# Kernel tuning notes

Measured on AMD Instinct MI355X. Metric: run time of the kernel, lower is better.

The kernel has to match this reference:

```python
import jax, jax.numpy as jnp
import numpy as np

B, N, T, D = 4, 170, 96, 256
H, HD = 8, 32          # num_heads, head_dim
TD, HIST, P = 24, 3, 16  # traffic_dim, history_size, num_patterns


def setup_inputs() -> dict:
    key = jax.random.key(0)
    ks = jax.random.split(key, 15)
    s = 0.02
    return {
        "query": jax.random.normal(ks[0], (B, N, T, D), jnp.float32),
        "key": jax.random.normal(ks[1], (B, N, T, D), jnp.float32),
        "value": jax.random.normal(ks[2], (B, N, T, D), jnp.float32),
        "pattern_matrix": jax.random.normal(ks[3], (P, HIST, TD), jnp.float32),
        "Wp": jax.random.normal(ks[4], (TD, TD), jnp.float32) * s,
        "bp": jnp.zeros((TD,), jnp.float32),
        "Wq": jax.random.normal(ks[5], (D, D), jnp.float32) * s,
        "bq": jnp.zeros((D,), jnp.float32),
        "Wk": jax.random.normal(ks[6], (D, D), jnp.float32) * s,
        "bk": jnp.zeros((D,), jnp.float32),
        "Wv": jax.random.normal(ks[7], (D, D), jnp.float32) * s,
        "bv": jnp.zeros((D,), jnp.float32),
        "Wo": jax.random.normal(ks[8], (D, D), jnp.float32) * s,
        "bo": jnp.zeros((D,), jnp.float32),
    }


def _forward(query, key, value, pattern_matrix, Wp, bp, Wq, bq, Wk, bk, Wv, bv, Wo, bo):
    b, n, t, d = query.shape
    # ---- compute_similarity: sliding windows over the traffic features ----
    tf = query[..., :TD]  # [B,N,T,TD]
    L = t - HIST + 1
    # windows[b,n,l,j,c] = tf[b,n,l+j,c]  (same as F.unfold with kernel (HIST,1))
    windows = jnp.stack([tf[:, :, j:j + L, :] for j in range(HIST)], axis=3)  # [B,N,L,HIST,TD]
    history_pattern = pattern_matrix @ Wp.T + bp  # [P,HIST,TD]
    # einsum('bhd,phd->bph') then mean over h == einsum over d, sum over h / HIST
    sim = jnp.einsum('bnlhd,phd->bnlp', windows, history_pattern) / HIST  # [B,N,L,P]
    pad = (HIST - 1) // 2
    sim = jnp.pad(sim, ((0, 0), (0, 0), (pad, pad), (0, 0)))  # [B,N,T,P]

    # ---- generate_temporal_mask ----
    sim_mean = sim.mean(axis=1)  # [B,T,P]
    temporal_weights = jax.nn.softmax(sim_mean, axis=-1).sum(axis=-1, keepdims=True)  # [B,T,1]
    tmask = temporal_weights @ jnp.swapaxes(temporal_weights, 1, 2)  # [B,T,T]
    # expand to [B,H,N,T,T] then flatten (torch indexing: b*H+h)
    mask_flat = jnp.broadcast_to(tmask[:, None, None, :, :], (b, H, n, t, t)).reshape(b * H, n, t, t)

    # ---- projections + head split (torch split/cat -> head-major batch: h*B+b) ----
    q = query @ Wq.T + bq
    k = key @ Wk.T + bk
    v = value @ Wv.T + bv
    def split_heads(x):
        return x.reshape(b, n, t, H, HD).transpose(3, 0, 1, 2, 4).reshape(H * b, n, t, HD)
    q, k, v = split_heads(q), split_heads(k), split_heads(v)

    scores = jnp.einsum('anqd,ankd->anqk', q, k) / jnp.sqrt(jnp.float32(HD))  # [H*B,N,T,T]
    scores = scores * mask_flat  # elementwise (shapes match; torch mixes head/batch order the same way)
    attn = jax.nn.softmax(scores, axis=-1)  # dropout is identity in eval mode
    out = jnp.einsum('anqk,ankd->anqd', attn, v)  # [H*B,N,T,HD]
    out = out.reshape(H, b, n, t, HD).transpose(1, 2, 3, 0, 4).reshape(b, n, t, d)
    return out @ Wo.T + bo


def reference(query, key, value, pattern_matrix, Wp, bp, Wq, bq, Wk, bk, Wv, bv, Wo, bo):
    return _forward(query, key, value, pattern_matrix, Wp, bp, Wq, bq, Wk, bk, Wv, bv, Wo, bo)
```

## Files before the change

### kernel.cpp

```cpp
#include <hip/hip_runtime.h>
#include <math.h>

#define B_  4
#define N_  170
#define T_  96
#define D_  256
#define H_  8
#define HD_ 32
#define BN_ (B_*N_)
#define WSZ (D_*D_)

typedef short  bf16x8 __attribute__((ext_vector_type(8)));
typedef float  f32x4  __attribute__((ext_vector_type(4)));

#define XB   0
#define KB   49152
#define VB   98304
#define LDSZ 147456

__device__ __forceinline__ ushort to_bf16(float x)
{
    uint u = __builtin_bit_cast(uint, x);
    u += 0x8000u;
    return (ushort)(u >> 16);
}

__device__ __forceinline__ uint pack2(float x0, float x1)
{
    return (uint)to_bf16(x0) | ((uint)to_bf16(x1) << 16);
}

__device__ __forceinline__ uint4 pack8(float4 a0, float4 a1)
{
    uint4 r;
    r.x = pack2(a0.x, a0.y); r.y = pack2(a0.z, a0.w);
    r.z = pack2(a1.x, a1.y); r.w = pack2(a1.z, a1.w);
    return r;
}

#define MFMA(a, b, c) __builtin_amdgcn_mfma_f32_16x16x32_bf16((a), (b), (c), 0, 0, 0)

__global__ __launch_bounds__(256)
void splitw_kernel(const float* __restrict__ Wq, const float* __restrict__ Wk,
                   const float* __restrict__ Wv, const float* __restrict__ Wo,
                   ushort* __restrict__ whi)
{
    const int gid = blockIdx.x * 256 + threadIdx.x;
    const int mat = gid >> 13;
    const int rem = gid & 8191;
    const int col = rem >> 5;
    const int kc  = rem & 31;
    const float* W = (mat == 0) ? Wq : (mat == 1) ? Wk : (mat == 2) ? Wv : Wo;
    const float s  = (mat == 0) ? 0.17677669529663687f : 1.0f;
    const float* p = W + (size_t)col * D_ + kc * 8;
    float4 a0 = *(const float4*)p;
    float4 a1 = *(const float4*)(p + 4);
    a0.x *= s; a0.y *= s; a0.z *= s; a0.w *= s;
    a1.x *= s; a1.y *= s; a1.z *= s; a1.w *= s;
    const size_t off = (size_t)mat * WSZ + ((size_t)kc * 256 + col) * 8;
    *(uint4*)(whi + off) = pack8(a0, a1);
}

__global__ __launch_bounds__(1024)
void mega_kernel(const float* __restrict__ Xq, const float* __restrict__ Xk,
                 const float* __restrict__ Xv, const ushort* __restrict__ W,
                 const float* __restrict__ bq, const float* __restrict__ bk,
                 const float* __restrict__ bv, const float* __restrict__ bo,
                 float* __restrict__ out)
{
    __shared__ __align__(16) char lds[LDSZ];

    const int bn   = blockIdx.x;
    const int tid  = threadIdx.x;
    const int wv   = tid >> 6;
    const int lane = tid & 63;
    const int lr   = lane & 15;
    const int kgl  = lane >> 4;
    const int h    = wv >> 1;
    const int ib   = (wv & 1) * 3;
    const size_t xoff = (size_t)bn * T_ * D_;

    int srow[3], skc[3]; uint saddr[3];
    #pragma unroll
    for (int c = 0; c < 3; c++) {
        const int cc = tid + c * 1024;
        const int row = cc % 96, kc = cc / 96;
        srow[c] = row; skc[c] = kc;
        saddr[c] = (uint)(((((kc >> 2) * 6 + (row >> 4)) * 4 + (kc & 3)) * 256)
                          + (row & 15) * 16);
    }

    #pragma unroll
    for (int c = 0; c < 3; c++) {
        const float* p = Xq + xoff + srow[c] * D_ + skc[c] * 8;
        float4 a0 = *(const float4*)p, a1 = *(const float4*)(p + 4);
        *(uint4*)(lds + XB + saddr[c]) = pack8(a0, a1);
    }
    __syncthreads();

    float4 pf[6];
    #pragma unroll
    for (int c = 0; c < 3; c++) {
        const float* p = Xk + xoff + srow[c] * D_ + skc[c] * 8;
        pf[2*c] = *(const float4*)p; pf[2*c+1] = *(const float4*)(p + 4);
    }

    {
        bf16x8 wf[8];
        #pragma unroll
        for (int ks = 0; ks < 8; ks++)
            wf[ks] = *(const bf16x8*)(W + ((size_t)(ks*4+kgl)*256 + wv*16 + lr)*8);
        f32x4 acc[6];
        #pragma unroll
        for (int nt = 0; nt < 6; nt++) acc[nt] = (f32x4)0.f;
        #pragma unroll
        for (int ks = 0; ks < 8; ks++)
            #pragma unroll
            for (int nt = 0; nt < 6; nt++) {
                bf16x8 xb = *(const bf16x8*)(lds + XB + ((ks*6+nt)*4+kgl)*256 + lr*16);
                acc[nt] = MFMA(wf[ks], xb, acc[nt]);
            }
        const float qs = 0.17677669529663687f;
        const int kg = (wv & 1)*2 + (kgl >> 1);
        float4 b4 = *(const float4*)(bq + wv*16 + kgl*4);
        #pragma unroll
        for (int nt = 0; nt < 6; nt++) {
            ushort4 o;
            o.x = to_bf16(acc[nt][0] + b4.x*qs);
            o.y = to_bf16(acc[nt][1] + b4.y*qs);
            o.z = to_bf16(acc[nt][2] + b4.z*qs);
            o.w = to_bf16(acc[nt][3] + b4.w*qs);
            *(ushort4*)(lds + VB + ((h*6+nt)*4+kg)*256 + lr*16 + (kgl&1)*8) = o;
        }
    }
    __syncthreads();

    #pragma unroll
    for (int c = 0; c < 3; c++)
        *(uint4*)(lds + XB + saddr[c]) = pack8(pf[2*c], pf[2*c+1]);
    bf16x8 qf[3];
    #pragma unroll
    for (int j = 0; j < 3; j++)
        qf[j] = *(const bf16x8*)(lds + VB + ((h*6 + ib + j)*4 + kgl)*256 + lr*16);
    #pragma unroll
    for (int c = 0; c < 3; c++) {
        const float* p = Xv + xoff + srow[c] * D_ + skc[c] * 8;
        pf[2*c] = *(const float4*)p; pf[2*c+1] = *(const float4*)(p + 4);
    }
    __syncthreads();

    {
        const ushort* Wk = W + WSZ;
        bf16x8 wf[8];
        #pragma unroll
        for (int ks = 0; ks < 8; ks++)
            wf[ks] = *(const bf16x8*)(Wk + ((size_t)(ks*4+kgl)*256 + wv*16 + lr)*8);
        f32x4 acc[6];
        #pragma unroll
        for (int nt = 0; nt < 6; nt++) acc[nt] = (f32x4)0.f;
        #pragma unroll
        for (int ks = 0; ks < 8; ks++)
            #pragma unroll
            for (int nt = 0; nt < 6; nt++) {
                bf16x8 xb = *(const bf16x8*)(lds + XB + ((ks*6+nt)*4+kgl)*256 + lr*16);
                acc[nt] = MFMA(wf[ks], xb, acc[nt]);
            }
        const int kg = (wv & 1)*2 + (kgl >> 1);
        float4 b4 = *(const float4*)(bk + wv*16 + kgl*4);
        #pragma unroll
        for (int nt = 0; nt < 6; nt++) {
            ushort4 o;
            o.x = to_bf16(acc[nt][0] + b4.x);
            o.y = to_bf16(acc[nt][1] + b4.y);
            o.z = to_bf16(acc[nt][2] + b4.z);
            o.w = to_bf16(acc[nt][3] + b4.w);
            *(ushort4*)(lds + KB + ((h*6+nt)*4+kg)*256 + lr*16 + (kgl&1)*8) = o;
        }
    }
    __syncthreads();

    #pragma unroll
    for (int c = 0; c < 3; c++)
        *(uint4*)(lds + XB + saddr[c]) = pack8(pf[2*c], pf[2*c+1]);
    __syncthreads();

    {
        const ushort* Wv = W + 2*WSZ;
        bf16x8 wf[8];
        #pragma unroll
        for (int ks = 0; ks < 8; ks++)
            wf[ks] = *(const bf16x8*)(Wv + ((size_t)(ks*4+kgl)*256 + wv*16 + lr)*8);
        f32x4 av[6];
        #pragma unroll
        for (int mt = 0; mt < 6; mt++) av[mt] = (f32x4)0.f;
        #pragma unroll
        for (int ks = 0; ks < 8; ks++)
            #pragma unroll
            for (int mt = 0; mt < 6; mt++) {
                bf16x8 xa = *(const bf16x8*)(lds + XB + ((ks*6+mt)*4+kgl)*256 + lr*16);
                av[mt] = MFMA(xa, wf[ks], av[mt]);
            }
        const int n2v = wv & 1;
        const float bvv = bv[wv*16 + lr];
        #pragma unroll
        for (int mt = 0; mt < 6; mt++) {
            const int kvkg = mt*2 + (kgl >> 1);
            const int s2 = kvkg >> 2, kgv = kvkg & 3;
            ushort4 o;
            o.x = to_bf16(av[mt][0] + bvv);
            o.y = to_bf16(av[mt][1] + bvv);
            o.z = to_bf16(av[mt][2] + bvv);
            o.w = to_bf16(av[mt][3] + bvv);
            *(ushort4*)(lds + VB + (((h*3+s2)*2+n2v)*4+kgv)*256 + lr*16 + (kgl&1)*8) = o;
        }
    }
    __syncthreads();

    f32x4 oacc[3][2];
    #pragma unroll
    for (int j = 0; j < 3; j++) { oacc[j][0] = (f32x4)0.f; oacc[j][1] = (f32x4)0.f; }
    {
        char* sw = lds + XB + wv * 3072;
        #pragma unroll
        for (int j = 0; j < 3; j++) {
            f32x4 s[6];
            #pragma unroll
            for (int mt = 0; mt < 6; mt++) {
                bf16x8 kf = *(const bf16x8*)(lds + KB + ((h*6+mt)*4+kgl)*256 + lr*16);
                s[mt] = MFMA(kf, qf[j], (f32x4)0.f);
            }
            float mx = s[0][0];
            #pragma unroll
            for (int mt = 0; mt < 6; mt++)
                #pragma unroll
                for (int r = 0; r < 4; r++) mx = fmaxf(mx, s[mt][r]);
            mx = fmaxf(mx, __shfl_xor(mx, 16));
            mx = fmaxf(mx, __shfl_xor(mx, 32));
            float sum = 0.f;
            #pragma unroll
            for (int mt = 0; mt < 6; mt++)
                #pragma unroll
                for (int r = 0; r < 4; r++) {
                    float e = __expf(s[mt][r] - mx);
                    s[mt][r] = e; sum += e;
                }
            sum += __shfl_xor(sum, 16);
            sum += __shfl_xor(sum, 32);
            const float inv = 1.f / sum;
            #pragma unroll
            for (int mt = 0; mt < 6; mt++) {
                uint2 u2;
                u2.x = pack2(s[mt][0]*inv, s[mt][1]*inv);
                u2.y = pack2(s[mt][2]*inv, s[mt][3]*inv);
                *(uint2*)(sw + (mt*2 + (kgl>>1))*256 + lr*16 + (kgl&1)*8) = u2;
            }
            #pragma unroll
            for (int s2 = 0; s2 < 3; s2++) {
                bf16x8 pa = *(const bf16x8*)(sw + (s2*4+kgl)*256 + lr*16);
                #pragma unroll
                for (int n2 = 0; n2 < 2; n2++) {
                    bf16x8 vf = *(const bf16x8*)(lds + VB + (((h*3+s2)*2+n2)*4+kgl)*256 + lr*16);
                    oacc[j][n2] = MFMA(pa, vf, oacc[j][n2]);
                }
            }
        }
    }
    __syncthreads();

    #pragma unroll
    for (int j = 0; j < 3; j++)
        #pragma unroll
        for (int n2 = 0; n2 < 2; n2++) {
            const int dcol = h*32 + n2*16 + lr;
            const int kc   = dcol >> 3;
            const int irow = ib + j;
            char* base = lds + XB + (((kc>>2)*6 + irow)*4 + (kc&3))*256 + (dcol&7)*2;
            #pragma unroll
            for (int r = 0; r < 4; r++)
                *(ushort*)(base + (kgl*4+r)*16) = to_bf16(oacc[j][n2][r]);
        }
    __syncthreads();

    {
        const ushort* Wo = W + 3*WSZ;
        bf16x8 wf[8];
        #pragma unroll
        for (int ks = 0; ks < 8; ks++)
            wf[ks] = *(const bf16x8*)(Wo + ((size_t)(ks*4+kgl)*256 + wv*16 + lr)*8);
        f32x4 a2[6];
        #pragma unroll
        for (int mt = 0; mt < 6; mt++) a2[mt] = (f32x4)0.f;
        #pragma unroll
        for (int ks = 0; ks < 8; ks++)
            #pragma unroll
            for (int mt = 0; mt < 6; mt++) {
                bf16x8 oa = *(const bf16x8*)(lds + XB + ((ks*6+mt)*4+kgl)*256 + lr*16);
                a2[mt] = MFMA(oa, wf[ks], a2[mt]);
            }
        const float bod = bo[wv*16 + lr];
        #pragma unroll
        for (int mt = 0; mt < 6; mt++)
            #pragma unroll
            for (int r = 0; r < 4; r++) {
                const int t = mt*16 + kgl*4 + r;
                out[((size_t)(bn*T_ + t))*D_ + wv*16 + lr] = a2[mt][r] + bod;
            }
    }
}

extern "C" void kernel_launch(void* const* d_in, const int* in_sizes, int n_in,
                              void* d_out, int out_size, void* d_ws, size_t ws_size,
                              hipStream_t stream)
{
    const float* query = (const float*)d_in[0];
    const float* key   = (const float*)d_in[1];
    const float* value = (const float*)d_in[2];
    const float* Wq = (const float*)d_in[6];
    const float* bq = (const float*)d_in[7];
    const float* Wk = (const float*)d_in[8];
    const float* bk = (const float*)d_in[9];
    const float* Wv = (const float*)d_in[10];
    const float* bv = (const float*)d_in[11];
    const float* Wo = (const float*)d_in[12];
    const float* bo = (const float*)d_in[13];

    float*  out = (float*)d_out;
    ushort* whi = (ushort*)d_ws;

    splitw_kernel<<<dim3(128), 256, 0, stream>>>(Wq, Wk, Wv, Wo, whi);
    mega_kernel<<<dim3(BN_), 1024, 0, stream>>>(
        query, key, value, whi, bq, bk, bv, bo, out);
}
```

Measured before the change: 101.6 us.

## Retile projection GEMMs into 2x3 per-wave blocks and hoist K fragments

Each wave now computes a 32-column by 48-row block (two weight column tiles times three row tiles) instead of a 16-column by 96-row strip in all four projection GEMMs. Every LDS activation fragment is reused for two MFMAs, which halves LDS reads per MFMA. In exchange the global weight fragments are reloaded per k-step instead of preloaded as eight registers. The attention stage also hoists the six K fragments out of the query-tile loop so they are read from LDS once instead of three times.

Result: slower. 111.8 us (+10.0%).

```diff
diff --git a/kernel.cpp b/kernel.cpp
--- a/kernel.cpp
+++ b/kernel.cpp
@@ -76,8 +76,9 @@
     const int lane = tid & 63;
     const int lr   = lane & 15;
     const int kgl  = lane >> 4;
-    const int h    = wv >> 1;
-    const int ib   = (wv & 1) * 3;
+    const int dp   = wv >> 1;
+    const int th   = wv & 1;
+    const int ib   = th * 3;
     const size_t xoff = (size_t)bn * T_ * D_;
 
     int srow[3], skc[3]; uint saddr[3];
@@ -106,31 +107,38 @@
     }
 
     {
-        bf16x8 wf[8];
-        #pragma unroll
-        for (int ks = 0; ks < 8; ks++)
-            wf[ks] = *(const bf16x8*)(W + ((size_t)(ks*4+kgl)*256 + wv*16 + lr)*8);
-        f32x4 acc[6];
-        #pragma unroll
-        for (int nt = 0; nt < 6; nt++) acc[nt] = (f32x4)0.f;
-        #pragma unroll
-        for (int ks = 0; ks < 8; ks++)
-            #pragma unroll
-            for (int nt = 0; nt < 6; nt++) {
-                bf16x8 xb = *(const bf16x8*)(lds + XB + ((ks*6+nt)*4+kgl)*256 + lr*16);
-                acc[nt] = MFMA(wf[ks], xb, acc[nt]);
-            }
+        f32x4 acc[2][3];
+        #pragma unroll
+        for (int u = 0; u < 2; u++)
+            #pragma unroll
+            for (int v = 0; v < 3; v++) acc[u][v] = (f32x4)0.f;
+        #pragma unroll
+        for (int ks = 0; ks < 8; ks++) {
+            bf16x8 w0 = *(const bf16x8*)(W + ((size_t)(ks*4+kgl)*256 + (dp*2+0)*16 + lr)*8);
+            bf16x8 w1 = *(const bf16x8*)(W + ((size_t)(ks*4+kgl)*256 + (dp*2+1)*16 + lr)*8);
+            #pragma unroll
+            for (int v = 0; v < 3; v++) {
+                bf16x8 xb = *(const bf16x8*)(lds + XB + ((ks*6 + th*3 + v)*4+kgl)*256 + lr*16);
+                acc[0][v] = MFMA(w0, xb, acc[0][v]);
+                acc[1][v] = MFMA(w1, xb, acc[1][v]);
+            }
+        }
         const float qs = 0.17677669529663687f;
-        const int kg = (wv & 1)*2 + (kgl >> 1);
-        float4 b4 = *(const float4*)(bq + wv*16 + kgl*4);
-        #pragma unroll
-        for (int nt = 0; nt < 6; nt++) {
-            ushort4 o;
-            o.x = to_bf16(acc[nt][0] + b4.x*qs);
-            o.y = to_bf16(acc[nt][1] + b4.y*qs);
-            o.z = to_bf16(acc[nt][2] + b4.z*qs);
-            o.w = to_bf16(acc[nt][3] + b4.w*qs);
-            *(ushort4*)(lds + VB + ((h*6+nt)*4+kg)*256 + lr*16 + (kgl&1)*8) = o;
+        #pragma unroll
+        for (int u = 0; u < 2; u++) {
+            const int mt = dp*2 + u;
+            const int kg = u*2 + (kgl >> 1);
+            float4 b4 = *(const float4*)(bq + mt*16 + kgl*4);
+            #pragma unroll
+            for (int v = 0; v < 3; v++) {
+                const int nt = th*3 + v;
+                ushort4 o;
+                o.x = to_bf16(acc[u][v][0] + b4.x*qs);
+                o.y = to_bf16(acc[u][v][1] + b4.y*qs);
+                o.z = to_bf16(acc[u][v][2] + b4.z*qs);
+                o.w = to_bf16(acc[u][v][3] + b4.w*qs);
+                *(ushort4*)(lds + VB + ((dp*6+nt)*4+kg)*256 + lr*16 + (kgl&1)*8) = o;
+            }
         }
     }
     __syncthreads();
@@ -141,7 +149,7 @@
     bf16x8 qf[3];
     #pragma unroll
     for (int j = 0; j < 3; j++)
-        qf[j] = *(const bf16x8*)(lds + VB + ((h*6 + ib + j)*4 + kgl)*256 + lr*16);
+        qf[j] = *(const bf16x8*)(lds + VB + ((dp*6 + ib + j)*4 + kgl)*256 + lr*16);
     #pragma unroll
     for (int c = 0; c < 3; c++) {
         const float* p = Xv + xoff + srow[c] * D_ + skc[c] * 8;
@@ -151,30 +159,37 @@
 
     {
         const ushort* Wk = W + WSZ;
-        bf16x8 wf[8];
-        #pragma unroll
-        for (int ks = 0; ks < 8; ks++)
-            wf[ks] = *(const bf16x8*)(Wk + ((size_t)(ks*4+kgl)*256 + wv*16 + lr)*8);
-        f32x4 acc[6];
-        #pragma unroll
-        for (int nt = 0; nt < 6; nt++) acc[nt] = (f32x4)0.f;
-        #pragma unroll
-        for (int ks = 0; ks < 8; ks++)
-            #pragma unroll
-            for (int nt = 0; nt < 6; nt++) {
-                bf16x8 xb = *(const bf16x8*)(lds + XB + ((ks*6+nt)*4+kgl)*256 + lr*16);
-                acc[nt] = MFMA(wf[ks], xb, acc[nt]);
-            }
-        const int kg = (wv & 1)*2 + (kgl >> 1);
-        float4 b4 = *(const float4*)(bk + wv*16 + kgl*4);
-        #pragma unroll
-        for (int nt = 0; nt < 6; nt++) {
-            ushort4 o;
-            o.x = to_bf16(acc[nt][0] + b4.x);
-            o.y = to_bf16(acc[nt][1] + b4.y);
-            o.z = to_bf16(acc[nt][2] + b4.z);
-            o.w = to_bf16(acc[nt][3] + b4.w);
-            *(ushort4*)(lds + KB + ((h*6+nt)*4+kg)*256 + lr*16 + (kgl&1)*8) = o;
+        f32x4 acc[2][3];
+        #pragma unroll
+        for (int u = 0; u < 2; u++)
+            #pragma unroll
+            for (int v = 0; v < 3; v++) acc[u][v] = (f32x4)0.f;
+        #pragma unroll
+        for (int ks = 0; ks < 8; ks++) {
+            bf16x8 w0 = *(const bf16x8*)(Wk + ((size_t)(ks*4+kgl)*256 + (dp*2+0)*16 + lr)*8);
+            bf16x8 w1 = *(const bf16x8*)(Wk + ((size_t)(ks*4+kgl)*256 + (dp*2+1)*16 + lr)*8);
+            #pragma unroll
+            for (int v = 0; v < 3; v++) {
+                bf16x8 xb = *(const bf16x8*)(lds + XB + ((ks*6 + th*3 + v)*4+kgl)*256 + lr*16);
+                acc[0][v] = MFMA(w0, xb, acc[0][v]);
+                acc[1][v] = MFMA(w1, xb, acc[1][v]);
+            }
+        }
+        #pragma unroll
+        for (int u = 0; u < 2; u++) {
+            const int mt = dp*2 + u;
+            const int kg = u*2 + (kgl >> 1);
+            float4 b4 = *(const float4*)(bk + mt*16 + kgl*4);
+            #pragma unroll
+            for (int v = 0; v < 3; v++) {
+                const int nt = th*3 + v;
+                ushort4 o;
+                o.x = to_bf16(acc[u][v][0] + b4.x);
+                o.y = to_bf16(acc[u][v][1] + b4.y);
+                o.z = to_bf16(acc[u][v][2] + b4.z);
+                o.w = to_bf16(acc[u][v][3] + b4.w);
+                *(ushort4*)(lds + KB + ((dp*6+nt)*4+kg)*256 + lr*16 + (kgl&1)*8) = o;
+            }
         }
     }
     __syncthreads();
@@ -186,32 +201,37 @@
 
     {
         const ushort* Wv = W + 2*WSZ;
-        bf16x8 wf[8];
-        #pragma unroll
-        for (int ks = 0; ks < 8; ks++)
-            wf[ks] = *(const bf16x8*)(Wv + ((size_t)(ks*4+kgl)*256 + wv*16 + lr)*8);
-        f32x4 av[6];
-        #pragma unroll
-        for (int mt = 0; mt < 6; mt++) av[mt] = (f32x4)0.f;
-        #pragma unroll
-        for (int ks = 0; ks < 8; ks++)
-            #pragma unroll
-            for (int mt = 0; mt < 6; mt++) {
-                bf16x8 xa = *(const bf16x8*)(lds + XB + ((ks*6+mt)*4+kgl)*256 + lr*16);
-                av[mt] = MFMA(xa, wf[ks], av[mt]);
-            }
-        const int n2v = wv & 1;
-        const float bvv = bv[wv*16 + lr];
-        #pragma unroll
-        for (int mt = 0; mt < 6; mt++) {
-            const int kvkg = mt*2 + (kgl >> 1);
-            const int s2 = kvkg >> 2, kgv = kvkg & 3;
-            ushort4 o;
-            o.x = to_bf16(av[mt][0] + bvv);
-            o.y = to_bf16(av[mt][1] + bvv);
-            o.z = to_bf16(av[mt][2] + bvv);
-            o.w = to_bf16(av[mt][3] + bvv);
-            *(ushort4*)(lds + VB + (((h*3+s2)*2+n2v)*4+kgv)*256 + lr*16 + (kgl&1)*8) = o;
+        f32x4 av[2][3];
+        #pragma unroll
+        for (int u = 0; u < 2; u++)
+            #pragma unroll
+            for (int v = 0; v < 3; v++) av[u][v] = (f32x4)0.f;
+        #pragma unroll
+        for (int ks = 0; ks < 8; ks++) {
+            bf16x8 w0 = *(const bf16x8*)(Wv + ((size_t)(ks*4+kgl)*256 + (dp*2+0)*16 + lr)*8);
+            bf16x8 w1 = *(const bf16x8*)(Wv + ((size_t)(ks*4+kgl)*256 + (dp*2+1)*16 + lr)*8);
+            #pragma unroll
+            for (int v = 0; v < 3; v++) {
+                bf16x8 xa = *(const bf16x8*)(lds + XB + ((ks*6 + th*3 + v)*4+kgl)*256 + lr*16);
+                av[0][v] = MFMA(xa, w0, av[0][v]);
+                av[1][v] = MFMA(xa, w1, av[1][v]);
+            }
+        }
+        #pragma unroll
+        for (int u = 0; u < 2; u++) {
+            const float bvv = bv[(dp*2+u)*16 + lr];
+            #pragma unroll
+            for (int v = 0; v < 3; v++) {
+                const int mt = th*3 + v;
+                const int kvkg = mt*2 + (kgl >> 1);
+                const int s2 = kvkg >> 2, kgv = kvkg & 3;
+                ushort4 o;
+                o.x = to_bf16(av[u][v][0] + bvv);
+                o.y = to_bf16(av[u][v][1] + bvv);
+                o.z = to_bf16(av[u][v][2] + bvv);
+                o.w = to_bf16(av[u][v][3] + bvv);
+                *(ushort4*)(lds + VB + (((dp*3+s2)*2+u)*4+kgv)*256 + lr*16 + (kgl&1)*8) = o;
+            }
         }
     }
     __syncthreads();
@@ -221,14 +241,16 @@
     for (int j = 0; j < 3; j++) { oacc[j][0] = (f32x4)0.f; oacc[j][1] = (f32x4)0.f; }
     {
         char* sw = lds + XB + wv * 3072;
+        bf16x8 kf[6];
+        #pragma unroll
+        for (int mt = 0; mt < 6; mt++)
+            kf[mt] = *(const bf16x8*)(lds + KB + ((dp*6+mt)*4+kgl)*256 + lr*16);
         #pragma unroll
         for (int j = 0; j < 3; j++) {
             f32x4 s[6];
             #pragma unroll
-            for (int mt = 0; mt < 6; mt++) {
-                bf16x8 kf = *(const bf16x8*)(lds + KB + ((h*6+mt)*4+kgl)*256 + lr*16);
-                s[mt] = MFMA(kf, qf[j], (f32x4)0.f);
-            }
+            for (int mt = 0; mt < 6; mt++)
+                s[mt] = MFMA(kf[mt], qf[j], (f32x4)0.f);
             float mx = s[0][0];
             #pragma unroll
             for (int mt = 0; mt < 6; mt++)
@@ -259,7 +281,7 @@
                 bf16x8 pa = *(const bf16x8*)(sw + (s2*4+kgl)*256 + lr*16);
                 #pragma unroll
                 for (int n2 = 0; n2 < 2; n2++) {
-                    bf16x8 vf = *(const bf16x8*)(lds + VB + (((h*3+s2)*2+n2)*4+kgl)*256 + lr*16);
+                    bf16x8 vf = *(const bf16x8*)(lds + VB + (((dp*3+s2)*2+n2)*4+kgl)*256 + lr*16);
                     oacc[j][n2] = MFMA(pa, vf, oacc[j][n2]);
                 }
             }
@@ -271,7 +293,7 @@
     for (int j = 0; j < 3; j++)
         #pragma unroll
         for (int n2 = 0; n2 < 2; n2++) {
-            const int dcol = h*32 + n2*16 + lr;
+            const int dcol = dp*32 + n2*16 + lr;
             const int kc   = dcol >> 3;
             const int irow = ib + j;
             char* base = lds + XB + (((kc>>2)*6 + irow)*4 + (kc&3))*256 + (dcol&7)*2;
@@ -283,28 +305,36 @@
 
     {
         const ushort* Wo = W + 3*WSZ;
-        bf16x8 wf[8];
-        #pragma unroll
-        for (int ks = 0; ks < 8; ks++)
-            wf[ks] = *(const bf16x8*)(Wo + ((size_t)(ks*4+kgl)*256 + wv*16 + lr)*8);
-        f32x4 a2[6];
-        #pragma unroll
-        for (int mt = 0; mt < 6; mt++) a2[mt] = (f32x4)0.f;
-        #pragma unroll
-        for (int ks = 0; ks < 8; ks++)
-            #pragma unroll
-            for (int mt = 0; mt < 6; mt++) {
-                bf16x8 oa = *(const bf16x8*)(lds + XB + ((ks*6+mt)*4+kgl)*256 + lr*16);
-                a2[mt] = MFMA(oa, wf[ks], a2[mt]);
-            }
-        const float bod = bo[wv*16 + lr];
-        #pragma unroll
-        for (int mt = 0; mt < 6; mt++)
-            #pragma unroll
-            for (int r = 0; r < 4; r++) {
-                const int t = mt*16 + kgl*4 + r;
-                out[((size_t)(bn*T_ + t))*D_ + wv*16 + lr] = a2[mt][r] + bod;
-            }
+        f32x4 a2[2][3];
+        #pragma unroll
+        for (int u = 0; u < 2; u++)
+            #pragma unroll
+            for (int v = 0; v < 3; v++) a2[u][v] = (f32x4)0.f;
+        #pragma unroll
+        for (int ks = 0; ks < 8; ks++) {
+            bf16x8 w0 = *(const bf16x8*)(Wo + ((size_t)(ks*4+kgl)*256 + (dp*2+0)*16 + lr)*8);
+            bf16x8 w1 = *(const bf16x8*)(Wo + ((size_t)(ks*4+kgl)*256 + (dp*2+1)*16 + lr)*8);
+            #pragma unroll
+            for (int v = 0; v < 3; v++) {
+                bf16x8 oa = *(const bf16x8*)(lds + XB + ((ks*6 + th*3 + v)*4+kgl)*256 + lr*16);
+                a2[0][v] = MFMA(oa, w0, a2[0][v]);
+                a2[1][v] = MFMA(oa, w1, a2[1][v]);
+            }
+        }
+        #pragma unroll
+        for (int u = 0; u < 2; u++) {
+            const int col = (dp*2+u)*16 + lr;
+            const float bod = bo[col];
+            #pragma unroll
+            for (int v = 0; v < 3; v++) {
+                const int mt = th*3 + v;
+                #pragma unroll
+                for (int r = 0; r < 4; r++) {
+                    const int t = mt*16 + kgl*4 + r;
+                    out[((size_t)(bn*T_ + t))*D_ + col] = a2[u][v][r] + bod;
+                }
+            }
+        }
     }
 }
 
```
